# Kernel optimization log

Measured on AMD Instinct MI355X. Metric: run time of the kernel, lower is better.

Reference implementation:

```python
import jax, jax.numpy as jnp
import numpy as np

N = 100000   # nodes
E = 1600000  # edges (avg degree 16)
D = 128      # in_dim


def setup_inputs() -> dict:
    key = jax.random.key(0)
    k = jax.random.split(key, 8)
    h = jax.random.normal(k[0], (N, D), dtype=jnp.float32)
    d = jax.random.uniform(k[1], (N,), dtype=jnp.float32)  # per-node degree norm (e.g. deg^-0.5)
    yes_no = jax.random.uniform(k[2], (E,), dtype=jnp.float32)
    gate_w = jax.random.normal(k[3], (1, 2 * D), dtype=jnp.float32) * (1.414 / np.sqrt(2 * D))
    gate_b = jnp.zeros((1,), dtype=jnp.float32)
    yes_weight = jax.random.uniform(k[4], (), dtype=jnp.float32)
    no_weight = jax.random.uniform(k[5], (), dtype=jnp.float32)
    src = jax.random.randint(k[6], (E,), 0, N, dtype=jnp.int64)
    dst = jax.random.randint(k[7], (E,), 0, N, dtype=jnp.int64)
    return {"h": h, "d": d, "yes_no": yes_no, "gate_w": gate_w, "gate_b": gate_b,
            "yes_weight": yes_weight, "no_weight": no_weight, "src": src, "dst": dst}


def reference(h, d, yes_no, gate_w, gate_b, yes_weight, no_weight, src, dst):
    n, dim = h.shape
    # gate(cat[h_dst, h_src]) == h_dst @ W[:, :D].T + h_src @ W[:, D:].T + b
    # project once per node, then gather per edge (avoids [E, 2D] concat)
    p_dst = h @ gate_w[0, :dim]  # [N]
    p_src = h @ gate_w[0, dim:]  # [N]
    g = jnp.tanh(p_dst[dst] + p_src[src] + gate_b[0])  # [E]
    yn = jnp.tanh(yes_no * yes_weight + (1.0 - yes_no) * no_weight)  # [E]
    e = (g + yn) * 0.5 * d[dst] * d[src]  # [E] (dropout p=0 -> identity)
    m = h[src] * e[:, None]  # [E, D] edge messages
    z = jax.ops.segment_sum(m, dst, num_segments=n)  # [N, D]
    return z
```

## Files before the change

kernel.cpp:

```cpp
#include <hip/hip_runtime.h>

#define D 128
#define CAP 64
#define NPB 250
#define NBMAX 512
#define EPB 4096
#define BCAP 5120

__device__ __forceinline__ unsigned short f2bf(float x) {
    unsigned int u = __float_as_uint(x);
    u += 0x7FFFu + ((u >> 16) & 1u);
    return (unsigned short)(u >> 16);
}
__device__ __forceinline__ float bf2f(unsigned short b) {
    return __uint_as_float(((unsigned int)b) << 16);
}

__global__ __launch_bounds__(256) void proj_kernel(const float* __restrict__ h,
                                                   const float* __restrict__ gw,
                                                   const float* __restrict__ dnorm,
                                                   float4* __restrict__ q,
                                                   unsigned short* __restrict__ hb,
                                                   unsigned int* __restrict__ tails,
                                                   int n_nodes) {
    if (blockIdx.x == 0) {
        tails[threadIdx.x] = 0u;
        tails[threadIdx.x + 256] = 0u;
    }
    int node = (int)((blockIdx.x * blockDim.x + threadIdx.x) >> 6);
    int lane = threadIdx.x & 63;
    if (node >= n_nodes) return;
    const float2* hr2 = (const float2*)(h + (size_t)node * D);
    const float2* gw2 = (const float2*)gw;
    float2 hv = hr2[lane];
    float2 wa = gw2[lane];
    float2 wb = gw2[lane + 64];
    ushort2 hvb = make_ushort2(f2bf(hv.x), f2bf(hv.y));
    *(ushort2*)(hb + (size_t)node * D + 2 * lane) = hvb;
    float s1 = hv.x * wa.x + hv.y * wa.y;
    float s2 = hv.x * wb.x + hv.y * wb.y;
    #pragma unroll
    for (int off = 32; off > 0; off >>= 1) {
        s1 += __shfl_down(s1, off, 64);
        s2 += __shfl_down(s2, off, 64);
    }
    if (lane == 0) q[node] = make_float4(s1, s2, dnorm[node], 0.0f);
}

__global__ __launch_bounds__(512) void bin_kernel(const float4* __restrict__ q,
                                                  const float* __restrict__ yes_no,
                                                  const int* __restrict__ src,
                                                  const int* __restrict__ dst,
                                                  const float* __restrict__ gate_b,
                                                  const float* __restrict__ yes_w,
                                                  const float* __restrict__ no_w,
                                                  unsigned int* __restrict__ tails,
                                                  unsigned long long* __restrict__ recs,
                                                  int n_edges, int nb) {
    __shared__ unsigned long long sorted[EPB];
    __shared__ unsigned int hist[NBMAX];
    __shared__ unsigned int sbuf[NBMAX];
    __shared__ unsigned int base[NBMAX];
    __shared__ unsigned int cursor[NBMAX];
    __shared__ unsigned int gbase[NBMAX];

    int tid = threadIdx.x;
    int e0 = blockIdx.x * EPB;
    int n = n_edges - e0;
    if (n > EPB) n = EPB;

    hist[tid] = 0u;
    __syncthreads();

    for (int j = tid; j < n; j += 512) {
        unsigned int d = (unsigned int)dst[e0 + j];
        atomicAdd(&hist[d / NPB], 1u);
    }
    __syncthreads();

    sbuf[tid] = hist[tid];
    __syncthreads();
    unsigned int* pa = sbuf;
    unsigned int* pb = gbase;
    #pragma unroll
    for (int s = 1; s < NBMAX; s <<= 1) {
        unsigned int v = pa[tid] + ((tid >= s) ? pa[tid - s] : 0u);
        pb[tid] = v;
        __syncthreads();
        unsigned int* t = pa; pa = pb; pb = t;
    }
    unsigned int ex = (tid == 0) ? 0u : pa[tid - 1];
    base[tid] = ex;
    cursor[tid] = ex;
    __syncthreads();

    float gb = gate_b[0];
    float yw = yes_w[0];
    float nw = no_w[0];

    for (int j = tid; j < n; j += 512) {
        int e = e0 + j;
        int dd = dst[e];
        int ss = src[e];
        float yn = yes_no[e];
        float4 qt = q[dd];
        float4 qs = q[ss];
        float g = tanhf(qt.x + qs.y + gb);
        float y = tanhf(yn * yw + (1.0f - yn) * nw);
        float ce = (g + y) * 0.5f * qt.z * qs.z;
        int qv = (int)rintf(ce * 8191.0f) + 8192;
        unsigned int w0 = ((unsigned int)ss << 15) | (unsigned int)qv;
        unsigned int bk = (unsigned int)dd / NPB;
        unsigned int pos = atomicAdd(&cursor[bk], 1u);
        sorted[pos] = ((unsigned long long)(unsigned int)dd << 32) | (unsigned long long)w0;
    }
    __syncthreads();

    gbase[tid] = (hist[tid] > 0u) ? atomicAdd(&tails[tid], hist[tid]) : 0u;
    __syncthreads();

    for (int j = tid; j < n; j += 512) {
        unsigned long long r = sorted[j];
        unsigned int bk = (unsigned int)(r >> 32) / NPB;
        unsigned int gpos = gbase[bk] + ((unsigned int)j - base[bk]);
        if (gpos < BCAP)
            __builtin_nontemporal_store(r, recs + (size_t)bk * BCAP + gpos);
    }
}

__global__ __launch_bounds__(256) void scatter_kernel(const unsigned int* __restrict__ tails,
                                                      const unsigned long long* __restrict__ recs,
                                                      int* __restrict__ cnt,
                                                      unsigned int* __restrict__ csr,
                                                      int n_nodes) {
    __shared__ unsigned int sw0[BCAP];
    __shared__ unsigned char snl[BCAP];
    __shared__ unsigned int hist2[256];
    __shared__ unsigned int sa[256];
    __shared__ unsigned int sb[256];
    __shared__ unsigned int rowbase[256];
    __shared__ unsigned int cursor2[256];

    int b = blockIdx.x;
    int tid = threadIdx.x;
    unsigned int nrec = tails[b];
    if (nrec > BCAP) nrec = BCAP;
    const unsigned long long* rb = recs + (size_t)b * BCAP;
    int node0 = b * NPB;

    hist2[tid] = 0u;
    __syncthreads();

    for (unsigned int j = tid; j < nrec; j += 256) {
        unsigned long long r = __builtin_nontemporal_load(rb + j);
        unsigned int nl = (unsigned int)(r >> 32) - (unsigned int)node0;
        atomicAdd(&hist2[nl], 1u);
    }
    __syncthreads();

    sa[tid] = hist2[tid];
    __syncthreads();
    unsigned int* pa = sa;
    unsigned int* pb = sb;
    #pragma unroll
    for (int s = 1; s < 256; s <<= 1) {
        unsigned int v = pa[tid] + ((tid >= s) ? pa[tid - s] : 0u);
        pb[tid] = v;
        __syncthreads();
        unsigned int* t = pa; pa = pb; pb = t;
    }
    unsigned int ex = (tid == 0) ? 0u : pa[tid - 1];
    rowbase[tid] = ex;
    cursor2[tid] = ex;
    __syncthreads();

    for (unsigned int j = tid; j < nrec; j += 256) {
        unsigned long long r = rb[j];
        unsigned int nl = (unsigned int)(r >> 32) - (unsigned int)node0;
        unsigned int pos = atomicAdd(&cursor2[nl], 1u);
        sw0[pos] = (unsigned int)r;
        snl[pos] = (unsigned char)nl;
    }
    __syncthreads();

    for (unsigned int j = tid; j < nrec; j += 256) {
        unsigned int nl = snl[j];
        unsigned int k = j - rowbase[nl];
        if (k < CAP)
            csr[(size_t)(node0 + (int)nl) * CAP + k] = sw0[j];
    }
    if (tid < NPB && node0 + tid < n_nodes)
        cnt[node0 + tid] = (int)hist2[tid];
}

__global__ __launch_bounds__(256) void gather_kernel(const unsigned short* __restrict__ hb,
                                                     const int* __restrict__ cnt,
                                                     const unsigned int* __restrict__ csr,
                                                     float4* __restrict__ z4,
                                                     int n_nodes) {
    int node = (int)((blockIdx.x * blockDim.x + threadIdx.x) >> 5);
    int lane = threadIdx.x & 31;
    if (node >= n_nodes) return;
    int n = cnt[node];
    if (n > CAP) n = CAP;
    const unsigned int* row = csr + (size_t)node * CAP;
    float4 acc = make_float4(0.0f, 0.0f, 0.0f, 0.0f);
    const float inv = 1.0f / 8191.0f;
    int k = 0;
    for (; k + 3 < n; k += 4) {
        unsigned int e0 = row[k], e1 = row[k + 1], e2 = row[k + 2], e3 = row[k + 3];
        float c0 = (float)((int)(e0 & 0x7fffu) - 8192) * inv;
        float c1 = (float)((int)(e1 & 0x7fffu) - 8192) * inv;
        float c2 = (float)((int)(e2 & 0x7fffu) - 8192) * inv;
        float c3 = (float)((int)(e3 & 0x7fffu) - 8192) * inv;
        ushort4 a = *(const ushort4*)(hb + (size_t)(e0 >> 15) * D + 4 * lane);
        ushort4 b = *(const ushort4*)(hb + (size_t)(e1 >> 15) * D + 4 * lane);
        ushort4 c = *(const ushort4*)(hb + (size_t)(e2 >> 15) * D + 4 * lane);
        ushort4 d = *(const ushort4*)(hb + (size_t)(e3 >> 15) * D + 4 * lane);
        acc.x += bf2f(a.x) * c0 + bf2f(b.x) * c1 + bf2f(c.x) * c2 + bf2f(d.x) * c3;
        acc.y += bf2f(a.y) * c0 + bf2f(b.y) * c1 + bf2f(c.y) * c2 + bf2f(d.y) * c3;
        acc.z += bf2f(a.z) * c0 + bf2f(b.z) * c1 + bf2f(c.z) * c2 + bf2f(d.z) * c3;
        acc.w += bf2f(a.w) * c0 + bf2f(b.w) * c1 + bf2f(c.w) * c2 + bf2f(d.w) * c3;
    }
    for (; k < n; ++k) {
        unsigned int e0 = row[k];
        float c0 = (float)((int)(e0 & 0x7fffu) - 8192) * inv;
        ushort4 a = *(const ushort4*)(hb + (size_t)(e0 >> 15) * D + 4 * lane);
        acc.x += bf2f(a.x) * c0;
        acc.y += bf2f(a.y) * c0;
        acc.z += bf2f(a.z) * c0;
        acc.w += bf2f(a.w) * c0;
    }
    z4[(size_t)node * (D / 4) + lane] = acc;
}

extern "C" void kernel_launch(void* const* d_in, const int* in_sizes, int n_in,
                              void* d_out, int out_size, void* d_ws, size_t ws_size,
                              hipStream_t stream) {
    const float* h       = (const float*)d_in[0];
    const float* dnorm   = (const float*)d_in[1];
    const float* yes_no  = (const float*)d_in[2];
    const float* gate_w  = (const float*)d_in[3];
    const float* gate_b  = (const float*)d_in[4];
    const float* yes_w   = (const float*)d_in[5];
    const float* no_w    = (const float*)d_in[6];
    const int*   src     = (const int*)d_in[7];
    const int*   dst     = (const int*)d_in[8];

    int n_nodes = in_sizes[0] / D;
    int n_edges = in_sizes[2];
    int nb = (n_nodes + NPB - 1) / NPB;

    char* ws = (char*)d_ws;
    size_t off = 0;
    auto take = [&](size_t bytes) {
        void* ptr = ws + off;
        off += (bytes + 15) & ~(size_t)15;
        return ptr;
    };
    float4*             q     = (float4*)take((size_t)n_nodes * sizeof(float4));
    unsigned short*     hb    = (unsigned short*)take((size_t)n_nodes * D * sizeof(unsigned short));
    int*                cnt   = (int*)take((size_t)n_nodes * sizeof(int));
    unsigned int*       csr   = (unsigned int*)take((size_t)n_nodes * CAP * sizeof(unsigned int));
    unsigned int*       tails = (unsigned int*)take((size_t)NBMAX * sizeof(unsigned int));
    unsigned long long* recs  = (unsigned long long*)take((size_t)nb * BCAP * sizeof(unsigned long long));
    (void)ws_size;

    proj_kernel<<<(n_nodes + 3) / 4, 256, 0, stream>>>(h, gate_w, dnorm, q, hb, tails, n_nodes);

    bin_kernel<<<(n_edges + EPB - 1) / EPB, 512, 0, stream>>>(
        q, yes_no, src, dst, gate_b, yes_w, no_w, tails, recs, n_edges, nb);

    scatter_kernel<<<nb, 256, 0, stream>>>(tails, recs, cnt, csr, n_nodes);

    gather_kernel<<<(n_nodes + 7) / 8, 256, 0, stream>>>(
        hb, cnt, csr, (float4*)d_out, n_nodes);
}
```

Measured before the change: 259.6 us.

## Slice bf16 features into column-major chunks and gather per slice

Stores the bf16 node features in 8 slices of 16 columns each, laid out slice-major, and launches the gather kernel with 8 blocks per 64-node group. Each block handles one slice, so the working set per slice (about 3.2 MB) can stay in L2/LLC during random source gathers. Also switches tanh to an exp/rcp approximation, halves edges per bin block, and uses nontemporal loads for the CSR rows. In exchange, CSR rows are re-read once per slice and each gather fetches only 8 bytes per lane.

```diff
diff --git a/kernel.cpp b/kernel.cpp
--- a/kernel.cpp
+++ b/kernel.cpp
@@ -4,8 +4,12 @@
 #define CAP 64
 #define NPB 250
 #define NBMAX 512
-#define EPB 4096
+#define EPB 2048
 #define BCAP 5120
+#define NSLICE 8
+#define SF 16
+
+typedef unsigned int u32x4 __attribute__((ext_vector_type(4)));
 
 __device__ __forceinline__ unsigned short f2bf(float x) {
     unsigned int u = __float_as_uint(x);
@@ -15,12 +19,16 @@
 __device__ __forceinline__ float bf2f(unsigned short b) {
     return __uint_as_float(((unsigned int)b) << 16);
 }
+__device__ __forceinline__ float fast_tanh(float x) {
+    float e = __expf(2.0f * x);
+    return 1.0f - 2.0f * __builtin_amdgcn_rcpf(e + 1.0f);
+}
 
 __global__ __launch_bounds__(256) void proj_kernel(const float* __restrict__ h,
                                                    const float* __restrict__ gw,
                                                    const float* __restrict__ dnorm,
                                                    float4* __restrict__ q,
-                                                   unsigned short* __restrict__ hb,
+                                                   unsigned short* __restrict__ hbt,
                                                    unsigned int* __restrict__ tails,
                                                    int n_nodes) {
     if (blockIdx.x == 0) {
@@ -36,7 +44,7 @@
     float2 wa = gw2[lane];
     float2 wb = gw2[lane + 64];
     ushort2 hvb = make_ushort2(f2bf(hv.x), f2bf(hv.y));
-    *(ushort2*)(hb + (size_t)node * D + 2 * lane) = hvb;
+    *(ushort2*)(hbt + ((size_t)(lane >> 3) * n_nodes + node) * SF + 2 * (lane & 7)) = hvb;
     float s1 = hv.x * wa.x + hv.y * wa.y;
     float s2 = hv.x * wb.x + hv.y * wb.y;
     #pragma unroll
@@ -105,8 +113,8 @@
         float yn = yes_no[e];
         float4 qt = q[dd];
         float4 qs = q[ss];
-        float g = tanhf(qt.x + qs.y + gb);
-        float y = tanhf(yn * yw + (1.0f - yn) * nw);
+        float g = fast_tanh(qt.x + qs.y + gb);
+        float y = fast_tanh(yn * yw + (1.0f - yn) * nw);
         float ce = (g + y) * 0.5f * qt.z * qs.z;
         int qv = (int)rintf(ce * 8191.0f) + 8192;
         unsigned int w0 = ((unsigned int)ss << 15) | (unsigned int)qv;
@@ -193,45 +201,47 @@
         cnt[node0 + tid] = (int)hist2[tid];
 }
 
-__global__ __launch_bounds__(256) void gather_kernel(const unsigned short* __restrict__ hb,
+__global__ __launch_bounds__(256) void gather_kernel(const unsigned short* __restrict__ hbt,
                                                      const int* __restrict__ cnt,
                                                      const unsigned int* __restrict__ csr,
-                                                     float4* __restrict__ z4,
+                                                     float* __restrict__ z,
                                                      int n_nodes) {
-    int node = (int)((blockIdx.x * blockDim.x + threadIdx.x) >> 5);
-    int lane = threadIdx.x & 31;
+    int slice = (int)(blockIdx.x & (NSLICE - 1));
+    int node  = (int)((blockIdx.x >> 3) * 64 + (threadIdx.x >> 2));
+    int ql    = (int)(threadIdx.x & 3);
     if (node >= n_nodes) return;
-    int n = cnt[node];
+    int n = __builtin_nontemporal_load(cnt + node);
     if (n > CAP) n = CAP;
     const unsigned int* row = csr + (size_t)node * CAP;
+    const unsigned short* hs = hbt + (size_t)slice * n_nodes * SF + 4 * ql;
     float4 acc = make_float4(0.0f, 0.0f, 0.0f, 0.0f);
     const float inv = 1.0f / 8191.0f;
     int k = 0;
     for (; k + 3 < n; k += 4) {
-        unsigned int e0 = row[k], e1 = row[k + 1], e2 = row[k + 2], e3 = row[k + 3];
-        float c0 = (float)((int)(e0 & 0x7fffu) - 8192) * inv;
-        float c1 = (float)((int)(e1 & 0x7fffu) - 8192) * inv;
-        float c2 = (float)((int)(e2 & 0x7fffu) - 8192) * inv;
-        float c3 = (float)((int)(e3 & 0x7fffu) - 8192) * inv;
-        ushort4 a = *(const ushort4*)(hb + (size_t)(e0 >> 15) * D + 4 * lane);
-        ushort4 b = *(const ushort4*)(hb + (size_t)(e1 >> 15) * D + 4 * lane);
-        ushort4 c = *(const ushort4*)(hb + (size_t)(e2 >> 15) * D + 4 * lane);
-        ushort4 d = *(const ushort4*)(hb + (size_t)(e3 >> 15) * D + 4 * lane);
+        u32x4 e = __builtin_nontemporal_load((const u32x4*)(row + k));
+        float c0 = (float)((int)(e.x & 0x7fffu) - 8192) * inv;
+        float c1 = (float)((int)(e.y & 0x7fffu) - 8192) * inv;
+        float c2 = (float)((int)(e.z & 0x7fffu) - 8192) * inv;
+        float c3 = (float)((int)(e.w & 0x7fffu) - 8192) * inv;
+        ushort4 a = *(const ushort4*)(hs + (size_t)(e.x >> 15) * SF);
+        ushort4 b = *(const ushort4*)(hs + (size_t)(e.y >> 15) * SF);
+        ushort4 c = *(const ushort4*)(hs + (size_t)(e.z >> 15) * SF);
+        ushort4 d = *(const ushort4*)(hs + (size_t)(e.w >> 15) * SF);
         acc.x += bf2f(a.x) * c0 + bf2f(b.x) * c1 + bf2f(c.x) * c2 + bf2f(d.x) * c3;
         acc.y += bf2f(a.y) * c0 + bf2f(b.y) * c1 + bf2f(c.y) * c2 + bf2f(d.y) * c3;
         acc.z += bf2f(a.z) * c0 + bf2f(b.z) * c1 + bf2f(c.z) * c2 + bf2f(d.z) * c3;
         acc.w += bf2f(a.w) * c0 + bf2f(b.w) * c1 + bf2f(c.w) * c2 + bf2f(d.w) * c3;
     }
     for (; k < n; ++k) {
-        unsigned int e0 = row[k];
+        unsigned int e0 = __builtin_nontemporal_load(row + k);
         float c0 = (float)((int)(e0 & 0x7fffu) - 8192) * inv;
-        ushort4 a = *(const ushort4*)(hb + (size_t)(e0 >> 15) * D + 4 * lane);
+        ushort4 a = *(const ushort4*)(hs + (size_t)(e0 >> 15) * SF);
         acc.x += bf2f(a.x) * c0;
         acc.y += bf2f(a.y) * c0;
         acc.z += bf2f(a.z) * c0;
         acc.w += bf2f(a.w) * c0;
     }
-    z4[(size_t)node * (D / 4) + lane] = acc;
+    *(float4*)(z + (size_t)node * D + slice * SF + 4 * ql) = acc;
 }
 
 extern "C" void kernel_launch(void* const* d_in, const int* in_sizes, int n_in,
@@ -259,20 +269,21 @@
         return ptr;
     };
     float4*             q     = (float4*)take((size_t)n_nodes * sizeof(float4));
-    unsigned short*     hb    = (unsigned short*)take((size_t)n_nodes * D * sizeof(unsigned short));
+    unsigned short*     hbt   = (unsigned short*)take((size_t)n_nodes * D * sizeof(unsigned short));
     int*                cnt   = (int*)take((size_t)n_nodes * sizeof(int));
     unsigned int*       csr   = (unsigned int*)take((size_t)n_nodes * CAP * sizeof(unsigned int));
     unsigned int*       tails = (unsigned int*)take((size_t)NBMAX * sizeof(unsigned int));
     unsigned long long* recs  = (unsigned long long*)take((size_t)nb * BCAP * sizeof(unsigned long long));
     (void)ws_size;
 
-    proj_kernel<<<(n_nodes + 3) / 4, 256, 0, stream>>>(h, gate_w, dnorm, q, hb, tails, n_nodes);
+    proj_kernel<<<(n_nodes + 3) / 4, 256, 0, stream>>>(h, gate_w, dnorm, q, hbt, tails, n_nodes);
 
     bin_kernel<<<(n_edges + EPB - 1) / EPB, 512, 0, stream>>>(
         q, yes_no, src, dst, gate_b, yes_w, no_w, tails, recs, n_edges, nb);
 
     scatter_kernel<<<nb, 256, 0, stream>>>(tails, recs, cnt, csr, n_nodes);
 
-    gather_kernel<<<(n_nodes + 7) / 8, 256, 0, stream>>>(
-        hb, cnt, csr, (float4*)d_out, n_nodes);
-}
+    int nodeblocks = (n_nodes + 63) / 64;
+    gather_kernel<<<nodeblocks * NSLICE, 256, 0, stream>>>(
+        hbt, cnt, csr, (float*)d_out, n_nodes);
+}
```

Result: slower. 373.5 us (+43.8%).
